# Performance work log

Measured on AMD Instinct MI355X. Metric: run time of the kernel, lower is better.

The kernel has to match this reference:

```python
import jax, jax.numpy as jnp
import numpy as np

H, LQ, LK, DK, DV = 16, 2048, 2048, 64, 64


def setup_inputs() -> dict:
    key = jax.random.key(0)
    k1, k2, k3, k4 = jax.random.split(key, 4)
    q = jax.random.normal(k1, (H, LQ, DK), dtype=jnp.float32)
    k = jax.random.normal(k2, (H, LK, DK), dtype=jnp.float32)
    v = jax.random.normal(k3, (1, LK, DV), dtype=jnp.float32)
    attn_mask = jax.random.randint(k4, (H, LQ, LK), 0, 2) == 1
    return {"q": q, "k": k, "v": v, "attn_mask": attn_mask, "train_attn": 1}


def reference(q, k, v, attn_mask, train_attn):
    scale = jnp.asarray(np.sqrt(q.shape[-1]), q.dtype)  # sqrt(d_k)
    # [H, Lq, Lk] scores
    attn = jnp.einsum('hqd,hkd->hqk', q, k) / scale
    attn = jnp.where(attn_mask, -jnp.inf, attn)
    attn = jax.nn.softmax(attn, axis=-1)
    # torch: v.repeat(n_heads,1,1) then bmm -> v[0] broadcast over heads
    attn_used = attn if train_attn else jax.lax.stop_gradient(attn)
    v_used = jax.lax.stop_gradient(v) if train_attn else v
    outputs = jnp.einsum('hqk,kd->hqd', attn_used, v_used[0])
    return outputs, attn
```

## Files before the change

### kernel.cpp

```cpp
#include <hip/hip_runtime.h>
#include <hip/hip_bf16.h>
#include <math.h>

#define H_ 16
#define LQ_ 2048
#define LK_ 2048
#define D_ 64
#define QB_ 16
#define NWAVE_ 16
#define COLSW_ 128
#define NT_ 8

using bf16x8  = __attribute__((ext_vector_type(8))) short;
using short4v = __attribute__((ext_vector_type(4))) short;
using floatx4 = __attribute__((ext_vector_type(4))) float;

__device__ __forceinline__ unsigned short f2bf(float x) {
  unsigned u = __builtin_bit_cast(unsigned, x);
  return (unsigned short)((u + 0x7fffu + ((u >> 16) & 1u)) >> 16);
}
__device__ __forceinline__ float bf2f(unsigned short b) {
  return __builtin_bit_cast(float, ((unsigned)b) << 16);
}
__device__ __forceinline__ void hilo8(const float* __restrict__ x, bf16x8& hv, bf16x8& lv) {
#pragma unroll
  for (int j = 0; j < 8; ++j) {
    unsigned short hb = f2bf(x[j]);
    float d = x[j] - bf2f(hb);
    hv[j] = (short)hb;
    lv[j] = (short)(unsigned short)(__builtin_bit_cast(unsigned, d) >> 16);
  }
}
__device__ __forceinline__ void hilo4(const float* __restrict__ x, short4v& hv, short4v& lv) {
#pragma unroll
  for (int j = 0; j < 4; ++j) {
    unsigned short hb = f2bf(x[j]);
    float d = x[j] - bf2f(hb);
    hv[j] = (short)hb;
    lv[j] = (short)(unsigned short)(__builtin_bit_cast(unsigned, d) >> 16);
  }
}

__device__ __forceinline__ floatx4 mfma32(bf16x8 a, bf16x8 b, floatx4 c) {
  return __builtin_amdgcn_mfma_f32_16x16x32_bf16(a, b, c, 0, 0, 0);
}
__device__ __forceinline__ floatx4 mfma16(short4v a, short4v b, floatx4 c) {
#if __has_builtin(__builtin_amdgcn_mfma_f32_16x16x16bf16_1k)
  return __builtin_amdgcn_mfma_f32_16x16x16bf16_1k(a, b, c, 0, 0, 0);
#else
  floatx4 d;
  asm("v_mfma_f32_16x16x16_bf16 %0, %1, %2, %3" : "=&v"(d) : "v"(a), "v"(b), "v"(c));
  return d;
#endif
}

__global__ void detect_mask_kernel(const unsigned* __restrict__ m, int* __restrict__ flag) {
  const int l = (int)threadIdx.x;
  unsigned acc = 0;
#pragma unroll
  for (int i = 0; i < 4; ++i) acc |= m[l * 4 + i];
  unsigned long long any = __ballot(acc & 0xFFFFFF00u);
  if (l == 0) *flag = any ? 1 : 0;
}

__global__ void pack_mask_kernel(const void* __restrict__ Mg, const int* __restrict__ flagp,
                                 unsigned* __restrict__ Wp) {
  const size_t i = (size_t)blockIdx.x * 256 + threadIdx.x;
  unsigned wbits = 0;
  if (*flagp) {
    const uint4* p = (const uint4*)((const unsigned char*)Mg + i * 32);
    uint4 a = p[0], b = p[1];
    unsigned v[8] = {a.x, a.y, a.z, a.w, b.x, b.y, b.z, b.w};
#pragma unroll
    for (int k = 0; k < 8; ++k)
#pragma unroll
      for (int bb = 0; bb < 4; ++bb)
        wbits |= (((v[k] >> (8 * bb)) & 0xFFu) ? 1u : 0u) << (4 * k + bb);
  } else {
    const uint4* p = (const uint4*)((const int*)Mg + i * 32);
#pragma unroll
    for (int k = 0; k < 8; ++k) {
      uint4 a = p[k];
      wbits |= (a.x ? 1u : 0u) << (4 * k)     | (a.y ? 1u : 0u) << (4 * k + 1) |
               (a.z ? 1u : 0u) << (4 * k + 2) | (a.w ? 1u : 0u) << (4 * k + 3);
    }
  }
  Wp[i] = wbits;
}

__global__ void conv_hilo_kernel(const float* __restrict__ X,
                                 unsigned short* __restrict__ Hh,
                                 unsigned short* __restrict__ Hl) {
  const size_t i = (size_t)blockIdx.x * 256 + threadIdx.x;
  float x[8];
  *(floatx4*)x       = *(const floatx4*)(X + i * 8);
  *(floatx4*)(x + 4) = *(const floatx4*)(X + i * 8 + 4);
  bf16x8 hv, lv;
  hilo8(x, hv, lv);
  *(bf16x8*)(Hh + i * 8) = hv;
  *(bf16x8*)(Hl + i * 8) = lv;
}

__global__ void conv_vt_kernel(const float* __restrict__ V,
                               unsigned short* __restrict__ Th,
                               unsigned short* __restrict__ Tl) {
  const int i = (int)(blockIdx.x * 256 + threadIdx.x);
  const int d = i >> 11, k = i & 2047;
  float x = V[(size_t)k * D_ + d];
  unsigned short hb = f2bf(x);
  float rem = x - bf2f(hb);
  Th[(size_t)d * LK_ + k] = hb;
  Tl[(size_t)d * LK_ + k] = (unsigned short)(__builtin_bit_cast(unsigned, rem) >> 16);
}

template <bool PRE>
__global__ __launch_bounds__(1024, 4)
void attn_v5_kernel(const float* __restrict__ Qg, const float* __restrict__ Kg,
                    const float* __restrict__ Vg, const void* __restrict__ Mg,
                    const int* __restrict__ flagp, const unsigned* __restrict__ Wp,
                    const unsigned short* __restrict__ Qhp, const unsigned short* __restrict__ Qlp,
                    const unsigned short* __restrict__ Khp, const unsigned short* __restrict__ Klp,
                    const unsigned short* __restrict__ Vthp, const unsigned short* __restrict__ Vtlp,
                    float* __restrict__ Og, float* __restrict__ Ag) {
  const int tid = (int)threadIdx.x;
  const int l = tid & 63, w = tid >> 6, lm = l & 15, lg = l >> 4;
  const int hd = (int)blockIdx.y;
  const int q0 = (int)blockIdx.x * QB_;
  const int k0 = w * COLSW_;

  __shared__ __align__(16) float OM[8][QB_ * D_];
  __shared__ float SmM[NWAVE_][QB_];
  __shared__ float SmS[NWAVE_][QB_];

  const int mB = PRE ? 0 : *flagp;
  const unsigned char* Mb = (const unsigned char*)Mg;
  const int* Mi = (const int*)Mg;
  const size_t qrow = (size_t)hd * LQ_ + q0 + lm;

  bf16x8 qh[2], ql[2];
  if constexpr (PRE) {
    const unsigned short* qp  = Qhp + qrow * D_;
    const unsigned short* qp2 = Qlp + qrow * D_;
    qh[0] = *(const bf16x8*)(qp  + lg * 8); qh[1] = *(const bf16x8*)(qp  + 32 + lg * 8);
    ql[0] = *(const bf16x8*)(qp2 + lg * 8); ql[1] = *(const bf16x8*)(qp2 + 32 + lg * 8);
  } else {
    const float* qp = Qg + qrow * D_;
#pragma unroll
    for (int s = 0; s < 2; ++s) {
      float x[8];
      *(floatx4*)x       = *(const floatx4*)(qp + s * 32 + lg * 8);
      *(floatx4*)(x + 4) = *(const floatx4*)(qp + s * 32 + lg * 8 + 4);
      hilo8(x, qh[s], ql[s]);
    }
  }

  unsigned wmv[4];
  if constexpr (PRE) {
#pragma unroll
    for (int i = 0; i < 4; ++i) wmv[i] = Wp[qrow * (LK_ / 32) + w * 4 + i];
  }

  float sc[NT_][4];
#pragma unroll
  for (int t = 0; t < NT_; ++t) {
    bf16x8 kh[2], kl[2];
    const size_t krow = (size_t)hd * LK_ + k0 + t * 16 + lm;
    if constexpr (PRE) {
      const unsigned short* kp  = Khp + krow * D_;
      const unsigned short* kp2 = Klp + krow * D_;
      kh[0] = *(const bf16x8*)(kp  + lg * 8); kh[1] = *(const bf16x8*)(kp  + 32 + lg * 8);
      kl[0] = *(const bf16x8*)(kp2 + lg * 8); kl[1] = *(const bf16x8*)(kp2 + 32 + lg * 8);
    } else {
      const float* kp = Kg + krow * D_;
#pragma unroll
      for (int s = 0; s < 2; ++s) {
        float x[8];
        *(floatx4*)x       = *(const floatx4*)(kp + s * 32 + lg * 8);
        *(floatx4*)(x + 4) = *(const floatx4*)(kp + s * 32 + lg * 8 + 4);
        hilo8(x, kh[s], kl[s]);
      }
    }
    floatx4 acc = {0.f, 0.f, 0.f, 0.f};
#pragma unroll
    for (int s = 0; s < 2; ++s) {
      acc = mfma32(kh[s], qh[s], acc);
      acc = mfma32(kl[s], qh[s], acc);
      acc = mfma32(kh[s], ql[s], acc);
    }
    if constexpr (PRE) {
#pragma unroll
      for (int j = 0; j < 4; ++j) {
        const int mk = (int)((wmv[t >> 1] >> ((t & 1) * 16 + lg * 4 + j)) & 1u);
        sc[t][j] = mk ? -1e30f : acc[j] * 0.125f;
      }
    } else if (mB) {
      const unsigned mw = *(const unsigned*)(Mb + qrow * LK_ + k0 + t * 16 + lg * 4);
#pragma unroll
      for (int j = 0; j < 4; ++j)
        sc[t][j] = ((mw >> (8 * j)) & 0xFFu) ? -1e30f : acc[j] * 0.125f;
    } else {
      const uint4 mv = *(const uint4*)(Mi + qrow * LK_ + k0 + t * 16 + lg * 4);
      const unsigned mm[4] = {mv.x, mv.y, mv.z, mv.w};
#pragma unroll
      for (int j = 0; j < 4; ++j) sc[t][j] = mm[j] ? -1e30f : acc[j] * 0.125f;
    }
  }

  float m = -1e30f;
#pragma unroll
  for (int t = 0; t < NT_; ++t)
#pragma unroll
    for (int j = 0; j < 4; ++j) m = fmaxf(m, sc[t][j]);
  m = fmaxf(m, __shfl_xor(m, 16, 64));
  m = fmaxf(m, __shfl_xor(m, 32, 64));
  if (lg == 0) SmM[w][lm] = m;
  __syncthreads();
  float mfin = SmM[0][lm];
#pragma unroll
  for (int ww = 1; ww < NWAVE_; ++ww) mfin = fmaxf(mfin, SmM[ww][lm]);

  float sum = 0.f;
#pragma unroll
  for (int t = 0; t < NT_; ++t)
#pragma unroll
    for (int j = 0; j < 4; ++j) {
      const float p = __expf(sc[t][j] - mfin);
      sc[t][j] = p;
      sum += p;
    }
  sum += __shfl_xor(sum, 16, 64);
  sum += __shfl_xor(sum, 32, 64);
  if (lg == 0) SmS[w][lm] = sum;
  __syncthreads();
  float tot = 0.f;
#pragma unroll
  for (int ww = 0; ww < NWAVE_; ++ww) tot += SmS[ww][lm];
  const float inv = 1.0f / tot;

  floatx4 oacc[4];
#pragma unroll
  for (int n = 0; n < 4; ++n) oacc[n] = {0.f, 0.f, 0.f, 0.f};

#pragma unroll
  for (int t = 0; t < NT_; ++t) {
    float p[4];
#pragma unroll
    for (int j = 0; j < 4; ++j) p[j] = sc[t][j] * inv;
    floatx4 pv = {p[0], p[1], p[2], p[3]};
    *(floatx4*)(Ag + qrow * LK_ + k0 + t * 16 + lg * 4) = pv;

    short4v ph, pl;
    hilo4(p, ph, pl);
#pragma unroll
    for (int n = 0; n < 4; ++n) {
      short4v vh, vl;
      if constexpr (PRE) {
        const size_t vo = (size_t)(n * 16 + lm) * LK_ + k0 + t * 16 + lg * 4;
        vh = *(const short4v*)(Vthp + vo);
        vl = *(const short4v*)(Vtlp + vo);
      } else {
        float vx[4];
#pragma unroll
        for (int j = 0; j < 4; ++j)
          vx[j] = Vg[(size_t)(k0 + t * 16 + lg * 4 + j) * D_ + n * 16 + lm];
        hilo4(vx, vh, vl);
      }
      floatx4 o = oacc[n];
      o = mfma16(ph, vh, o);
      o = mfma16(pl, vh, o);
      o = mfma16(ph, vl, o);
      oacc[n] = o;
    }
  }

  __syncthreads();
  if (w >= 8) {
#pragma unroll
    for (int n = 0; n < 4; ++n)
#pragma unroll
      for (int j = 0; j < 4; ++j)
        OM[w - 8][(lg * 4 + j) * D_ + n * 16 + lm] = oacc[n][j];
  }
  __syncthreads();
  if (w < 8) {
#pragma unroll
    for (int n = 0; n < 4; ++n)
#pragma unroll
      for (int j = 0; j < 4; ++j) {
        const int idx = (lg * 4 + j) * D_ + n * 16 + lm;
        OM[w][idx] += oacc[n][j];
      }
  }
  __syncthreads();
  {
    const int i = tid;
    float o = 0.f;
#pragma unroll
    for (int s = 0; s < 8; ++s) o += OM[s][i];
    Og[((size_t)hd * LQ_ + q0 + (i >> 6)) * D_ + (i & 63)] = o;
  }
}

extern "C" void kernel_launch(void* const* d_in, const int* in_sizes, int n_in,
                              void* d_out, int out_size, void* d_ws, size_t ws_size,
                              hipStream_t stream) {
  const float* Qg = (const float*)d_in[0];
  const float* Kg = (const float*)d_in[1];
  const float* Vg = (const float*)d_in[2];
  const void*  Mg = d_in[3];

  char* ws = (char*)d_ws;
  int* flag = (int*)ws;
  unsigned*       Wp  = (unsigned*)(ws + 16);
  unsigned short* Qhp = (unsigned short*)(ws + 16 + 8388608);
  unsigned short* Qlp = (unsigned short*)(ws + 16 + 8388608 + 4194304);
  unsigned short* Khp = (unsigned short*)(ws + 16 + 8388608 + 2 * 4194304);
  unsigned short* Klp = (unsigned short*)(ws + 16 + 8388608 + 3 * 4194304);
  unsigned short* Vth = (unsigned short*)(ws + 16 + 8388608 + 4 * 4194304);
  unsigned short* Vtl = (unsigned short*)(ws + 16 + 8388608 + 4 * 4194304 + 262144);
  const size_t WS_NEEDED = 16 + 8388608 + 4 * (size_t)4194304 + 2 * (size_t)262144;

  float* Og = (float*)d_out;
  float* Ag = (float*)d_out + (size_t)H_ * LQ_ * D_;

  hipLaunchKernelGGL(detect_mask_kernel, dim3(1), dim3(64), 0, stream,
                     (const unsigned*)Mg, flag);

  dim3 grid(LQ_ / QB_, H_);
  if (ws_size >= WS_NEEDED) {
    hipLaunchKernelGGL(pack_mask_kernel, dim3(8192), dim3(256), 0, stream, Mg, flag, Wp);
    hipLaunchKernelGGL(conv_hilo_kernel, dim3(1024), dim3(256), 0, stream, Qg, Qhp, Qlp);
    hipLaunchKernelGGL(conv_hilo_kernel, dim3(1024), dim3(256), 0, stream, Kg, Khp, Klp);
    hipLaunchKernelGGL(conv_vt_kernel, dim3(512), dim3(256), 0, stream, Vg, Vth, Vtl);
    hipLaunchKernelGGL((attn_v5_kernel<true>), grid, dim3(1024), 0, stream,
                       Qg, Kg, Vg, Mg, flag, Wp, Qhp, Qlp, Khp, Klp, Vth, Vtl, Og, Ag);
  } else {
    hipLaunchKernelGGL((attn_v5_kernel<false>), grid, dim3(1024), 0, stream,
                       Qg, Kg, Vg, Mg, flag, Wp, Qhp, Qlp, Khp, Klp, Vth, Vtl, Og, Ag);
  }
}
```

Baseline: 833.1 us.

## Halve waves per block, pair K tiles, pack V hi/lo, prescale Q

The attention kernel now uses 8 waves per block instead of 16, so each wave handles 256 key columns. K tiles are processed in pairs with interleaved MFMAs to raise instruction-level parallelism. The V hi/lo bf16 halves are packed into one 32-bit word so a single wide load fetches both. The 1/sqrt(d) scale is folded into the Q conversion pre-pass. The aim is to cut cross-wave reduction and per-tile overhead, at the cost of more registers per wave and fewer waves in flight.

```diff
diff --git a/kernel.cpp b/kernel.cpp
--- a/kernel.cpp
+++ b/kernel.cpp
@@ -7,9 +7,9 @@
 #define LK_ 2048
 #define D_ 64
 #define QB_ 16
-#define NWAVE_ 16
-#define COLSW_ 128
-#define NT_ 8
+#define NW_ 8
+#define COLSW_ 256
+#define NT_ 16
 
 using bf16x8  = __attribute__((ext_vector_type(8))) short;
 using short4v = __attribute__((ext_vector_type(4))) short;
@@ -90,37 +90,37 @@
 
 __global__ void conv_hilo_kernel(const float* __restrict__ X,
                                  unsigned short* __restrict__ Hh,
-                                 unsigned short* __restrict__ Hl) {
+                                 unsigned short* __restrict__ Hl, float scale) {
   const size_t i = (size_t)blockIdx.x * 256 + threadIdx.x;
   float x[8];
   *(floatx4*)x       = *(const floatx4*)(X + i * 8);
   *(floatx4*)(x + 4) = *(const floatx4*)(X + i * 8 + 4);
+#pragma unroll
+  for (int j = 0; j < 8; ++j) x[j] *= scale;
   bf16x8 hv, lv;
   hilo8(x, hv, lv);
   *(bf16x8*)(Hh + i * 8) = hv;
   *(bf16x8*)(Hl + i * 8) = lv;
 }
 
-__global__ void conv_vt_kernel(const float* __restrict__ V,
-                               unsigned short* __restrict__ Th,
-                               unsigned short* __restrict__ Tl) {
+__global__ void conv_vc_kernel(const float* __restrict__ V, unsigned* __restrict__ Vc) {
   const int i = (int)(blockIdx.x * 256 + threadIdx.x);
   const int d = i >> 11, k = i & 2047;
   float x = V[(size_t)k * D_ + d];
   unsigned short hb = f2bf(x);
   float rem = x - bf2f(hb);
-  Th[(size_t)d * LK_ + k] = hb;
-  Tl[(size_t)d * LK_ + k] = (unsigned short)(__builtin_bit_cast(unsigned, rem) >> 16);
+  unsigned short lb = (unsigned short)(__builtin_bit_cast(unsigned, rem) >> 16);
+  Vc[(size_t)d * LK_ + k] = (unsigned)hb | ((unsigned)lb << 16);
 }
 
 template <bool PRE>
-__global__ __launch_bounds__(1024, 4)
-void attn_v5_kernel(const float* __restrict__ Qg, const float* __restrict__ Kg,
+__global__ __launch_bounds__(512, 2)
+void attn_v7_kernel(const float* __restrict__ Qg, const float* __restrict__ Kg,
                     const float* __restrict__ Vg, const void* __restrict__ Mg,
                     const int* __restrict__ flagp, const unsigned* __restrict__ Wp,
                     const unsigned short* __restrict__ Qhp, const unsigned short* __restrict__ Qlp,
                     const unsigned short* __restrict__ Khp, const unsigned short* __restrict__ Klp,
-                    const unsigned short* __restrict__ Vthp, const unsigned short* __restrict__ Vtlp,
+                    const unsigned* __restrict__ Vcp,
                     float* __restrict__ Og, float* __restrict__ Ag) {
   const int tid = (int)threadIdx.x;
   const int l = tid & 63, w = tid >> 6, lm = l & 15, lg = l >> 4;
@@ -128,9 +128,9 @@
   const int q0 = (int)blockIdx.x * QB_;
   const int k0 = w * COLSW_;
 
-  __shared__ __align__(16) float OM[8][QB_ * D_];
-  __shared__ float SmM[NWAVE_][QB_];
-  __shared__ float SmS[NWAVE_][QB_];
+  __shared__ __align__(16) float OM[4][QB_ * D_];
+  __shared__ float SmM[NW_][QB_];
+  __shared__ float SmS[NW_][QB_];
 
   const int mB = PRE ? 0 : *flagp;
   const unsigned char* Mb = (const unsigned char*)Mg;
@@ -154,55 +154,78 @@
     }
   }
 
-  unsigned wmv[4];
+  unsigned wmv[8];
   if constexpr (PRE) {
 #pragma unroll
-    for (int i = 0; i < 4; ++i) wmv[i] = Wp[qrow * (LK_ / 32) + w * 4 + i];
+    for (int i = 0; i < 8; ++i) wmv[i] = Wp[qrow * (LK_ / 32) + w * 8 + i];
   }
 
   float sc[NT_][4];
 #pragma unroll
-  for (int t = 0; t < NT_; ++t) {
-    bf16x8 kh[2], kl[2];
-    const size_t krow = (size_t)hd * LK_ + k0 + t * 16 + lm;
+  for (int tp = 0; tp < NT_ / 2; ++tp) {
+    const int t0 = 2 * tp, t1 = 2 * tp + 1;
+    bf16x8 khA[2], klA[2], khB[2], klB[2];
+    const size_t krowA = (size_t)hd * LK_ + k0 + t0 * 16 + lm;
+    const size_t krowB = (size_t)hd * LK_ + k0 + t1 * 16 + lm;
     if constexpr (PRE) {
-      const unsigned short* kp  = Khp + krow * D_;
-      const unsigned short* kp2 = Klp + krow * D_;
-      kh[0] = *(const bf16x8*)(kp  + lg * 8); kh[1] = *(const bf16x8*)(kp  + 32 + lg * 8);
-      kl[0] = *(const bf16x8*)(kp2 + lg * 8); kl[1] = *(const bf16x8*)(kp2 + 32 + lg * 8);
+      const unsigned short* kpA  = Khp + krowA * D_;
+      const unsigned short* kpA2 = Klp + krowA * D_;
+      const unsigned short* kpB  = Khp + krowB * D_;
+      const unsigned short* kpB2 = Klp + krowB * D_;
+      khA[0] = *(const bf16x8*)(kpA  + lg * 8); khA[1] = *(const bf16x8*)(kpA  + 32 + lg * 8);
+      klA[0] = *(const bf16x8*)(kpA2 + lg * 8); klA[1] = *(const bf16x8*)(kpA2 + 32 + lg * 8);
+      khB[0] = *(const bf16x8*)(kpB  + lg * 8); khB[1] = *(const bf16x8*)(kpB  + 32 + lg * 8);
+      klB[0] = *(const bf16x8*)(kpB2 + lg * 8); klB[1] = *(const bf16x8*)(kpB2 + 32 + lg * 8);
     } else {
-      const float* kp = Kg + krow * D_;
+      const float* kpA = Kg + krowA * D_;
+      const float* kpB = Kg + krowB * D_;
 #pragma unroll
       for (int s = 0; s < 2; ++s) {
-        float x[8];
-        *(floatx4*)x       = *(const floatx4*)(kp + s * 32 + lg * 8);
-        *(floatx4*)(x + 4) = *(const floatx4*)(kp + s * 32 + lg * 8 + 4);
-        hilo8(x, kh[s], kl[s]);
-      }
-    }
-    floatx4 acc = {0.f, 0.f, 0.f, 0.f};
+        float xa[8], xb[8];
+        *(floatx4*)xa       = *(const floatx4*)(kpA + s * 32 + lg * 8);
+        *(floatx4*)(xa + 4) = *(const floatx4*)(kpA + s * 32 + lg * 8 + 4);
+        *(floatx4*)xb       = *(const floatx4*)(kpB + s * 32 + lg * 8);
+        *(floatx4*)(xb + 4) = *(const floatx4*)(kpB + s * 32 + lg * 8 + 4);
+        hilo8(xa, khA[s], klA[s]);
+        hilo8(xb, khB[s], klB[s]);
+      }
+    }
+    floatx4 accA = {0.f, 0.f, 0.f, 0.f};
+    floatx4 accB = {0.f, 0.f, 0.f, 0.f};
 #pragma unroll
     for (int s = 0; s < 2; ++s) {
-      acc = mfma32(kh[s], qh[s], acc);
-      acc = mfma32(kl[s], qh[s], acc);
-      acc = mfma32(kh[s], ql[s], acc);
+      accA = mfma32(khA[s], qh[s], accA);
+      accB = mfma32(khB[s], qh[s], accB);
+      accA = mfma32(klA[s], qh[s], accA);
+      accB = mfma32(klB[s], qh[s], accB);
+      accA = mfma32(khA[s], ql[s], accA);
+      accB = mfma32(khB[s], ql[s], accB);
     }
     if constexpr (PRE) {
+      const unsigned w0 = wmv[tp];
 #pragma unroll
       for (int j = 0; j < 4; ++j) {
-        const int mk = (int)((wmv[t >> 1] >> ((t & 1) * 16 + lg * 4 + j)) & 1u);
-        sc[t][j] = mk ? -1e30f : acc[j] * 0.125f;
+        sc[t0][j] = ((w0 >> (lg * 4 + j)) & 1u)        ? -1e30f : accA[j];
+        sc[t1][j] = ((w0 >> (16 + lg * 4 + j)) & 1u)   ? -1e30f : accB[j];
       }
     } else if (mB) {
-      const unsigned mw = *(const unsigned*)(Mb + qrow * LK_ + k0 + t * 16 + lg * 4);
-#pragma unroll
-      for (int j = 0; j < 4; ++j)
-        sc[t][j] = ((mw >> (8 * j)) & 0xFFu) ? -1e30f : acc[j] * 0.125f;
+      const unsigned mwA = *(const unsigned*)(Mb + qrow * LK_ + k0 + t0 * 16 + lg * 4);
+      const unsigned mwB = *(const unsigned*)(Mb + qrow * LK_ + k0 + t1 * 16 + lg * 4);
+#pragma unroll
+      for (int j = 0; j < 4; ++j) {
+        sc[t0][j] = ((mwA >> (8 * j)) & 0xFFu) ? -1e30f : accA[j] * 0.125f;
+        sc[t1][j] = ((mwB >> (8 * j)) & 0xFFu) ? -1e30f : accB[j] * 0.125f;
+      }
     } else {
-      const uint4 mv = *(const uint4*)(Mi + qrow * LK_ + k0 + t * 16 + lg * 4);
-      const unsigned mm[4] = {mv.x, mv.y, mv.z, mv.w};
-#pragma unroll
-      for (int j = 0; j < 4; ++j) sc[t][j] = mm[j] ? -1e30f : acc[j] * 0.125f;
+      const uint4 mvA = *(const uint4*)(Mi + qrow * LK_ + k0 + t0 * 16 + lg * 4);
+      const uint4 mvB = *(const uint4*)(Mi + qrow * LK_ + k0 + t1 * 16 + lg * 4);
+      const unsigned ma[4] = {mvA.x, mvA.y, mvA.z, mvA.w};
+      const unsigned mb2[4] = {mvB.x, mvB.y, mvB.z, mvB.w};
+#pragma unroll
+      for (int j = 0; j < 4; ++j) {
+        sc[t0][j] = ma[j]  ? -1e30f : accA[j] * 0.125f;
+        sc[t1][j] = mb2[j] ? -1e30f : accB[j] * 0.125f;
+      }
     }
   }
 
@@ -217,7 +240,7 @@
   __syncthreads();
   float mfin = SmM[0][lm];
 #pragma unroll
-  for (int ww = 1; ww < NWAVE_; ++ww) mfin = fmaxf(mfin, SmM[ww][lm]);
+  for (int ww = 1; ww < NW_; ++ww) mfin = fmaxf(mfin, SmM[ww][lm]);
 
   float sum = 0.f;
 #pragma unroll
@@ -234,7 +257,7 @@
   __syncthreads();
   float tot = 0.f;
 #pragma unroll
-  for (int ww = 0; ww < NWAVE_; ++ww) tot += SmS[ww][lm];
+  for (int ww = 0; ww < NW_; ++ww) tot += SmS[ww][lm];
   const float inv = 1.0f / tot;
 
   floatx4 oacc[4];
@@ -251,38 +274,55 @@
 
     short4v ph, pl;
     hilo4(p, ph, pl);
-#pragma unroll
-    for (int n = 0; n < 4; ++n) {
-      short4v vh, vl;
-      if constexpr (PRE) {
-        const size_t vo = (size_t)(n * 16 + lm) * LK_ + k0 + t * 16 + lg * 4;
-        vh = *(const short4v*)(Vthp + vo);
-        vl = *(const short4v*)(Vtlp + vo);
-      } else {
+
+    if constexpr (PRE) {
+      uint4 vw[4];
+#pragma unroll
+      for (int n = 0; n < 4; ++n)
+        vw[n] = *(const uint4*)(Vcp + (size_t)(n * 16 + lm) * LK_ + k0 + t * 16 + lg * 4);
+#pragma unroll
+      for (int n = 0; n < 4; ++n) {
+        short4v vh, vl;
+        const unsigned vv[4] = {vw[n].x, vw[n].y, vw[n].z, vw[n].w};
+#pragma unroll
+        for (int j = 0; j < 4; ++j) {
+          vh[j] = (short)(unsigned short)(vv[j] & 0xFFFFu);
+          vl[j] = (short)(unsigned short)(vv[j] >> 16);
+        }
+        floatx4 o = oacc[n];
+        o = mfma16(ph, vh, o);
+        o = mfma16(pl, vh, o);
+        o = mfma16(ph, vl, o);
+        oacc[n] = o;
+      }
+    } else {
+#pragma unroll
+      for (int n = 0; n < 4; ++n) {
         float vx[4];
 #pragma unroll
         for (int j = 0; j < 4; ++j)
           vx[j] = Vg[(size_t)(k0 + t * 16 + lg * 4 + j) * D_ + n * 16 + lm];
+        short4v vh, vl;
         hilo4(vx, vh, vl);
-      }
-      floatx4 o = oacc[n];
-      o = mfma16(ph, vh, o);
-      o = mfma16(pl, vh, o);
-      o = mfma16(ph, vl, o);
-      oacc[n] = o;
-    }
-  }
-
-  __syncthreads();
-  if (w >= 8) {
+        floatx4 o = oacc[n];
+        o = mfma16(ph, vh, o);
+        o = mfma16(pl, vh, o);
+        o = mfma16(ph, vl, o);
+        oacc[n] = o;
+      }
+    }
+  }
+
+  __syncthreads();
+  if (w >= 4) {
 #pragma unroll
     for (int n = 0; n < 4; ++n)
 #pragma unroll
       for (int j = 0; j < 4; ++j)
-        OM[w - 8][(lg * 4 + j) * D_ + n * 16 + lm] = oacc[n][j];
-  }
-  __syncthreads();
-  if (w < 8) {
+        OM[w - 4][(lg * 4 + j) * D_ + n * 16 + lm] = oacc[n][j];
+  }
+  __syncthreads();
+  if (w < 4) {
 #pragma unroll
     for (int n = 0; n < 4; ++n)
 #pragma unroll
@@ -292,11 +332,9 @@
       }
   }
   __syncthreads();
-  {
-    const int i = tid;
-    float o = 0.f;
-#pragma unroll
-    for (int s = 0; s < 8; ++s) o += OM[s][i];
+#pragma unroll
+  for (int i = tid; i < QB_ * D_; i += 512) {
+    const float o = OM[0][i] + OM[1][i] + OM[2][i] + OM[3][i];
     Og[((size_t)hd * LQ_ + q0 + (i >> 6)) * D_ + (i & 63)] = o;
   }
 }
@@ -316,9 +354,8 @@
   unsigned short* Qlp = (unsigned short*)(ws + 16 + 8388608 + 4194304);
   unsigned short* Khp = (unsigned short*)(ws + 16 + 8388608 + 2 * 4194304);
   unsigned short* Klp = (unsigned short*)(ws + 16 + 8388608 + 3 * 4194304);
-  unsigned short* Vth = (unsigned short*)(ws + 16 + 8388608 + 4 * 4194304);
-  unsigned short* Vtl = (unsigned short*)(ws + 16 + 8388608 + 4 * 4194304 + 262144);
-  const size_t WS_NEEDED = 16 + 8388608 + 4 * (size_t)4194304 + 2 * (size_t)262144;
+  unsigned*       Vcp = (unsigned*)(ws + 16 + 8388608 + 4 * 4194304);
+  const size_t WS_NEEDED = 16 + 8388608 + 4 * (size_t)4194304 + (size_t)524288;
 
   float* Og = (float*)d_out;
   float* Ag = (float*)d_out + (size_t)H_ * LQ_ * D_;
@@ -329,13 +366,13 @@
   dim3 grid(LQ_ / QB_, H_);
   if (ws_size >= WS_NEEDED) {
     hipLaunchKernelGGL(pack_mask_kernel, dim3(8192), dim3(256), 0, stream, Mg, flag, Wp);
-    hipLaunchKernelGGL(conv_hilo_kernel, dim3(1024), dim3(256), 0, stream, Qg, Qhp, Qlp);
-    hipLaunchKernelGGL(conv_hilo_kernel, dim3(1024), dim3(256), 0, stream, Kg, Khp, Klp);
-    hipLaunchKernelGGL(conv_vt_kernel, dim3(512), dim3(256), 0, stream, Vg, Vth, Vtl);
-    hipLaunchKernelGGL((attn_v5_kernel<true>), grid, dim3(1024), 0, stream,
-                       Qg, Kg, Vg, Mg, flag, Wp, Qhp, Qlp, Khp, Klp, Vth, Vtl, Og, Ag);
+    hipLaunchKernelGGL(conv_hilo_kernel, dim3(1024), dim3(256), 0, stream, Qg, Qhp, Qlp, 0.125f);
+    hipLaunchKernelGGL(conv_hilo_kernel, dim3(1024), dim3(256), 0, stream, Kg, Khp, Klp, 1.0f);
+    hipLaunchKernelGGL(conv_vc_kernel, dim3(512), dim3(256), 0, stream, Vg, Vcp);
+    hipLaunchKernelGGL((attn_v7_kernel<true>), grid, dim3(512), 0, stream,
+                       Qg, Kg, Vg, Mg, flag, Wp, Qhp, Qlp, Khp, Klp, Vcp, Og, Ag);
   } else {
-    hipLaunchKernelGGL((attn_v5_kernel<false>), grid, dim3(1024), 0, stream,
-                       Qg, Kg, Vg, Mg, flag, Wp, Qhp, Qlp, Khp, Klp, Vth, Vtl, Og, Ag);
-  }
-}
+    hipLaunchKernelGGL((attn_v7_kernel<false>), grid, dim3(512), 0, stream,
+                       Qg, Kg, Vg, Mg, flag, Wp, Qhp, Qlp, Khp, Klp, Vcp, Og, Ag);
+  }
+}
```

Measured after the change: 735.0 us. 1.13x faster.
